# Kernel optimization log

Measured on AMD Instinct MI355X. Metric: run time of the kernel, lower is better.

## Reference

```python
import jax, jax.numpy as jnp
import numpy as np

N_NODES = 262144
N_EDGES = 2097152
N_GRAPHS = 8192
IN_CH = 54
HID = 32
OUT_CH = 64
SLOPE = 0.01  # AttentiveFP uses leaky_relu / GATConv negative_slope=0.01
NUM_TIMESTEPS = 2


def _gru(x, h, wih, whh, bih, bhh):
    # torch.nn.GRUCell semantics
    gi = x @ wih.T + bih
    gh = h @ whh.T + bhh
    ir, iz, inn = jnp.split(gi, 3, axis=-1)
    hr, hz, hn = jnp.split(gh, 3, axis=-1)
    r = jax.nn.sigmoid(ir + hr)
    z = jax.nn.sigmoid(iz + hz)
    n = jnp.tanh(inn + r * hn)
    return (1.0 - z) * n + z * h


def _seg_softmax(a, idx, n):
    # PyG softmax over edges grouped by target index
    m = jax.ops.segment_max(a, idx, num_segments=n)
    e = jnp.exp(a - m[idx])
    s = jax.ops.segment_sum(e, idx, num_segments=n)
    return e / (s[idx] + 1e-16)


def _forward(x, edge_attr,
             lin1_w, lin1_b,
             g_lin1_w, g_lin2_w, g_att_l, g_att_r, g_bias,
             gru1_wih, gru1_whh, gru1_bih, gru1_bhh,
             a_lin_w, a_att_src, a_att_dst, a_bias,
             gru2_wih, gru2_whh, gru2_bih, gru2_bhh,
             m_lin_w, m_att_src, m_att_dst, m_bias,
             gru3_wih, gru3_whh, gru3_bih, gru3_bhh,
             lin2_w, lin2_b,
             edge_index, batch_index):
    src, dst = edge_index[0], edge_index[1]  # j -> i (source_to_target)
    n = x.shape[0]
    # Atom embedding
    x = jax.nn.leaky_relu(x @ lin1_w.T + lin1_b, SLOPE)
    # --- GATEConv (first layer, uses edge features) ---
    xj, xi = x[src], x[dst]
    e = jax.nn.leaky_relu(jnp.concatenate([xj, edge_attr], axis=-1) @ g_lin1_w.T, SLOPE)
    alpha = jax.nn.leaky_relu(e @ g_att_l + xi @ g_att_r, SLOPE)
    alpha = _seg_softmax(alpha, dst, n)
    h = jax.ops.segment_sum((xj @ g_lin2_w.T) * alpha[:, None], dst, num_segments=n) + g_bias
    h = jax.nn.elu(h)
    x = jax.nn.relu(_gru(h, x, gru1_wih, gru1_whh, gru1_bih, gru1_bhh))
    # --- GATConv atom layer (num_layers=2 -> one extra conv) ---
    xt = x @ a_lin_w.T
    al = xt @ a_att_src
    ar = xt @ a_att_dst
    alpha = jax.nn.leaky_relu(al[src] + ar[dst], SLOPE)
    alpha = _seg_softmax(alpha, dst, n)
    h = jax.ops.segment_sum(xt[src] * alpha[:, None], dst, num_segments=n) + a_bias
    h = jax.nn.elu(h)
    x = jax.nn.relu(_gru(h, x, gru2_wih, gru2_whh, gru2_bih, gru2_bhh))
    # --- Molecule readout: iterative GAT attention from nodes to their graph ---
    out = jax.nn.relu(jax.ops.segment_sum(x, batch_index, num_segments=N_GRAPHS))
    xs = x @ m_lin_w.T          # transformed node (source) features, fixed per step
    a_node = xs @ m_att_src     # per-node attention logit contribution
    for _ in range(NUM_TIMESTEPS):
        a_g = (out @ m_lin_w.T) @ m_att_dst  # per-graph contribution
        alpha = jax.nn.leaky_relu(a_node + a_g[batch_index], SLOPE)
        alpha = _seg_softmax(alpha, batch_index, N_GRAPHS)
        h = jax.ops.segment_sum(xs * alpha[:, None], batch_index, num_segments=N_GRAPHS) + m_bias
        h = jax.nn.elu(h)
        out = jax.nn.relu(_gru(h, out, gru3_wih, gru3_whh, gru3_bih, gru3_bhh))
    out = out @ lin2_w.T + lin2_b
    # Mish activation wrapper
    return out * jnp.tanh(jax.nn.softplus(out))


def setup_inputs() -> dict:
    key = jax.random.key(0)
    ks = jax.random.split(key, 24)
    def rn(k, shape, s=0.1):
        return jax.random.normal(k, shape, dtype=jnp.float32) * s
    z = lambda *s: jnp.zeros(s, jnp.float32)
    return {
        "x": jax.random.normal(ks[0], (N_NODES, IN_CH), dtype=jnp.float32),
        "edge_attr": jax.random.normal(ks[1], (N_EDGES, 1), dtype=jnp.float32),
        "edge_index": jax.random.randint(ks[2], (2, N_EDGES), 0, N_NODES, dtype=jnp.int32),
        "batch_index": jnp.sort(jax.random.randint(ks[3], (N_NODES,), 0, N_GRAPHS, dtype=jnp.int32)),
        "lin1_w": rn(ks[4], (HID, IN_CH)), "lin1_b": z(HID),
        "g_lin1_w": rn(ks[5], (HID, HID + 1)),
        "g_lin2_w": rn(ks[6], (HID, HID)),
        "g_att_l": rn(ks[7], (HID,)), "g_att_r": rn(ks[8], (HID,)),
        "g_bias": z(HID),
        "gru1_wih": rn(ks[9], (3 * HID, HID)), "gru1_whh": rn(ks[10], (3 * HID, HID)),
        "gru1_bih": z(3 * HID), "gru1_bhh": z(3 * HID),
        "a_lin_w": rn(ks[11], (HID, HID)),
        "a_att_src": rn(ks[12], (HID,)), "a_att_dst": rn(ks[13], (HID,)),
        "a_bias": z(HID),
        "gru2_wih": rn(ks[14], (3 * HID, HID)), "gru2_whh": rn(ks[15], (3 * HID, HID)),
        "gru2_bih": z(3 * HID), "gru2_bhh": z(3 * HID),
        "m_lin_w": rn(ks[16], (HID, HID)),
        "m_att_src": rn(ks[17], (HID,)), "m_att_dst": rn(ks[18], (HID,)),
        "m_bias": z(HID),
        "gru3_wih": rn(ks[19], (3 * HID, HID)), "gru3_whh": rn(ks[20], (3 * HID, HID)),
        "gru3_bih": z(3 * HID), "gru3_bhh": z(3 * HID),
        "lin2_w": rn(ks[21], (OUT_CH, HID)), "lin2_b": z(OUT_CH),
    }


def reference(x, edge_attr, edge_index, batch_index,
              lin1_w, lin1_b,
              g_lin1_w, g_lin2_w, g_att_l, g_att_r, g_bias,
              gru1_wih, gru1_whh, gru1_bih, gru1_bhh,
              a_lin_w, a_att_src, a_att_dst, a_bias,
              gru2_wih, gru2_whh, gru2_bih, gru2_bhh,
              m_lin_w, m_att_src, m_att_dst, m_bias,
              gru3_wih, gru3_whh, gru3_bih, gru3_bhh,
              lin2_w, lin2_b):
    return _forward(x, edge_attr,
                    lin1_w, lin1_b,
                    g_lin1_w, g_lin2_w, g_att_l, g_att_r, g_bias,
                    gru1_wih, gru1_whh, gru1_bih, gru1_bhh,
                    a_lin_w, a_att_src, a_att_dst, a_bias,
                    gru2_wih, gru2_whh, gru2_bih, gru2_bhh,
                    m_lin_w, m_att_src, m_att_dst, m_bias,
                    gru3_wih, gru3_whh, gru3_bih, gru3_bhh,
                    lin2_w, lin2_b,
                    edge_index, batch_index)
```

## Files before the change

### kernel.cpp

```cpp
#include <hip/hip_runtime.h>
#include <hip/hip_bf16.h>
#include <math.h>

#define NN 262144
#define NE 2097152
#define NG 8192
#define THREADS 256

typedef __hip_bfloat16 bf16;
typedef __attribute__((ext_vector_type(8))) short short8v;
typedef __attribute__((ext_vector_type(4))) float f32x4;

static __device__ __forceinline__ float lrelu(float x){ return x > 0.f ? x : 0.01f*x; }
static __device__ __forceinline__ float eluf(float x){ return x > 0.f ? x : __expf(x) - 1.f; }
static __device__ __forceinline__ float sigm(float x){ return 1.f/(1.f + __expf(-x)); }
static __device__ __forceinline__ float tanh_fast(float x){
  float e = __expf(2.f*x); return 1.f - 2.f/(e + 1.f);
}
static __device__ __forceinline__ float b2f(bf16 v){ return __bfloat162float(v); }
static __device__ __forceinline__ bf16 f2b(float v){ return __float2bfloat16(v); }
static __device__ __forceinline__ float s2f(short s){
  return __uint_as_float(((unsigned int)(unsigned short)s) << 16);
}

static __device__ __forceinline__ unsigned short bfbits(float f){
  union { bf16 b; unsigned short s; } u; u.b = f2b(f); return u.s;
}
static __device__ __forceinline__ unsigned int pack2(float lo, float hi){
  return (unsigned int)bfbits(lo) | ((unsigned int)bfbits(hi) << 16);
}

static __device__ __forceinline__ float redsum32(float t){
  #pragma unroll
  for (int o = 16; o > 0; o >>= 1) t += __shfl_xor(t, o, 32);
  return t;
}
static __device__ __forceinline__ float redmax32(float t){
  #pragma unroll
  for (int o = 16; o > 0; o >>= 1) t = fmaxf(t, __shfl_xor(t, o, 32));
  return t;
}

static __device__ __forceinline__ float gru_relu(float hv, float xv, int c,
    const float* __restrict__ wih, const float* __restrict__ whh,
    const float* __restrict__ bih, const float* __restrict__ bhh){
  float gr = bih[c], gz = bih[32+c], gn = bih[64+c];
  float hr = bhh[c], hz = bhh[32+c], hn = bhh[64+c];
  #pragma unroll 8
  for (int k = 0; k < 32; k++){
    float hk = __shfl(hv, k, 32);
    float xk = __shfl(xv, k, 32);
    gr += hk*wih[(     c)*32 + k];
    gz += hk*wih[(32 + c)*32 + k];
    gn += hk*wih[(64 + c)*32 + k];
    hr += xk*whh[(     c)*32 + k];
    hz += xk*whh[(32 + c)*32 + k];
    hn += xk*whh[(64 + c)*32 + k];
  }
  float r = sigm(gr + hr), z = sigm(gz + hz);
  float nn2 = tanh_fast(gn + r*hn);
  return fmaxf((1.f - z)*nn2 + z*xv, 0.f);
}

__global__ __launch_bounds__(THREADS) void k_filli(int* __restrict__ p, int v, int n){
  int i = blockIdx.x*THREADS + threadIdx.x;
  if (i < n) p[i] = v;
}

#define FB_EMBED 512
#define FB_HIST  8192
#define FB_GPTR  1024

__global__ __launch_bounds__(THREADS) void k_front(
    const float* __restrict__ xin, const float* __restrict__ lw, const float* __restrict__ lb,
    const float* __restrict__ w1, const float* __restrict__ w2,
    const float* __restrict__ attr_r, float* __restrict__ X,
    bf16* __restrict__ u, bf16* __restrict__ v, float* __restrict__ nr,
    const int* __restrict__ ei, int* __restrict__ hist, int* __restrict__ rank,
    const int* __restrict__ batch, int* __restrict__ gptr){
  __shared__ float ol[4][16][33];
  int bid = blockIdx.x;
  if (bid < FB_EMBED){
    int wid  = bid*4 + (threadIdx.x >> 6);
    int wv   = threadIdx.x >> 6;
    int lane = threadIdx.x & 63;
    int cl = lane & 15;
    int kb = lane >> 4;
    short8v BL[2][2], BU[2], BV[2];
    #pragma unroll
    for (int g = 0; g < 2; g++){
      #pragma unroll
      for (int kc = 0; kc < 2; kc++){
        short8v t;
        #pragma unroll
        for (int j = 0; j < 8; j++){
          int k = kc*32 + kb*8 + j;
          t[j] = (k < 54) ? (short)bfbits(lw[(size_t)(g*16+cl)*54 + k]) : (short)0;
        }
        BL[g][kc] = t;
      }
      short8v tu, tv;
      #pragma unroll
      for (int j = 0; j < 8; j++){
        tu[j] = (short)bfbits(w1[(size_t)(g*16+cl)*33 + kb*8 + j]);
        tv[j] = (short)bfbits(w2[(size_t)(g*16+cl)*32 + kb*8 + j]);
      }
      BU[g] = tu; BV[g] = tv;
    }
    float bb0 = lb[cl], bb1 = lb[16+cl];
    float ar0 = attr_r[cl], ar1 = attr_r[16+cl];
    f32x4 zero; zero[0]=0.f; zero[1]=0.f; zero[2]=0.f; zero[3]=0.f;

    for (int t = 0; t < 8; t++){
      int nb = (wid*8 + t)*16;
      const float* xrow = xin + (size_t)(nb + cl)*54;
      short8v Ax0, Ax1;
      const float2* x2 = (const float2*)(xrow + kb*8);
      #pragma unroll
      for (int jj = 0; jj < 4; jj++){
        float2 tvv = x2[jj];
        Ax0[2*jj]   = (short)bfbits(tvv.x);
        Ax0[2*jj+1] = (short)bfbits(tvv.y);
      }
      #pragma unroll
      for (int j = 0; j < 8; j++){
        int k = 32 + kb*8 + j;
        Ax1[j] = (k < 54) ? (short)bfbits(xrow[k]) : (short)0;
      }
      f32x4 a0, a1;
      #pragma unroll
      for (int q = 0; q < 4; q++){ a0[q] = bb0; a1[q] = bb1; }
      f32x4 d0 = __builtin_amdgcn_mfma_f32_16x16x32_bf16(Ax0, BL[0][0], a0, 0, 0, 0);
      d0 = __builtin_amdgcn_mfma_f32_16x16x32_bf16(Ax1, BL[0][1], d0, 0, 0, 0);
      f32x4 d1 = __builtin_amdgcn_mfma_f32_16x16x32_bf16(Ax0, BL[1][0], a1, 0, 0, 0);
      d1 = __builtin_amdgcn_mfma_f32_16x16x32_bf16(Ax1, BL[1][1], d1, 0, 0, 0);
      #pragma unroll
      for (int r = 0; r < 4; r++){ d0[r] = lrelu(d0[r]); d1[r] = lrelu(d1[r]); }
      #pragma unroll
      for (int r = 0; r < 4; r++){
        int node = nb + kb*4 + r;
        float* srow = X + (size_t)node*32;
        srow[cl]      = d0[r];
        srow[16 + cl] = d1[r];
        ol[wv][kb*4 + r][cl]      = d0[r];
        ol[wv][kb*4 + r][16 + cl] = d1[r];
      }
      #pragma unroll
      for (int r = 0; r < 4; r++){
        float vsum = d0[r]*ar0 + d1[r]*ar1;
        vsum += __shfl_xor(vsum, 1, 16);
        vsum += __shfl_xor(vsum, 2, 16);
        vsum += __shfl_xor(vsum, 4, 16);
        vsum += __shfl_xor(vsum, 8, 16);
        if (cl == 0) nr[nb + kb*4 + r] = vsum;
      }
      __syncthreads();
      short8v Ao;
      #pragma unroll
      for (int j = 0; j < 8; j++) Ao[j] = (short)bfbits(ol[wv][cl][kb*8 + j]);
      f32x4 u0 = __builtin_amdgcn_mfma_f32_16x16x32_bf16(Ao, BU[0], zero, 0, 0, 0);
      f32x4 u1 = __builtin_amdgcn_mfma_f32_16x16x32_bf16(Ao, BU[1], zero, 0, 0, 0);
      f32x4 v0 = __builtin_amdgcn_mfma_f32_16x16x32_bf16(Ao, BV[0], zero, 0, 0, 0);
      f32x4 v1 = __builtin_amdgcn_mfma_f32_16x16x32_bf16(Ao, BV[1], zero, 0, 0, 0);
      #pragma unroll
      for (int r = 0; r < 4; r++){
        int node = nb + kb*4 + r;
        bf16* ur = u + (size_t)node*32;
        bf16* vr = v + (size_t)node*32;
        ur[cl]      = f2b(u0[r]);
        ur[16 + cl] = f2b(u1[r]);
        vr[cl]      = f2b(v0[r]);
        vr[16 + cl] = f2b(v1[r]);
      }
      __syncthreads();
    }
  } else if (bid < FB_EMBED + FB_HIST){
    int e = (bid - FB_EMBED)*THREADS + threadIdx.x;
    rank[e] = atomicAdd(hist + ei[NE + e], 1);
  } else {
    int n = (bid - FB_EMBED - FB_HIST)*THREADS + threadIdx.x;
    int bc = batch[n];
    if (n == 0){ for (int g = 0; g <= bc; g++) gptr[g] = 0; }
    else {
      int pb = batch[n-1];
      if (pb != bc) for (int g = pb+1; g <= bc; g++) gptr[g] = n;
    }
    if (n == NN-1){ for (int g = bc+1; g <= NG; g++) gptr[g] = NN; }
  }
}

__global__ __launch_bounds__(THREADS) void k_scan1(const int* __restrict__ hist,
    int* __restrict__ rp1, int* __restrict__ btot){
  __shared__ int sh[THREADS];
  int i = blockIdx.x*THREADS + threadIdx.x;
  int v = hist[i];
  sh[threadIdx.x] = v; __syncthreads();
  #pragma unroll
  for (int off = 1; off < THREADS; off <<= 1){
    int t = (threadIdx.x >= off) ? sh[threadIdx.x - off] : 0;
    __syncthreads(); sh[threadIdx.x] += t; __syncthreads();
  }
  rp1[i] = sh[threadIdx.x] - v;
  if (threadIdx.x == THREADS-1) btot[blockIdx.x] = sh[THREADS-1];
}

__global__ __launch_bounds__(1024) void k_scan2(int* __restrict__ btot){
  __shared__ int sh[1024];
  int i = threadIdx.x;
  int v = btot[i];
  sh[i] = v; __syncthreads();
  for (int off = 1; off < 1024; off <<= 1){
    int t = (i >= off) ? sh[i - off] : 0;
    __syncthreads(); sh[i] += t; __syncthreads();
  }
  btot[i] = sh[i] - v;
}

#define MB_SCAN 1024

__global__ __launch_bounds__(THREADS) void k_mid(const int* __restrict__ rp1,
    const int* __restrict__ btot, int* __restrict__ rowptr,
    const int* __restrict__ ei, const float* __restrict__ ea,
    const int* __restrict__ rank, int2* __restrict__ epk){
  int bid = blockIdx.x;
  if (bid < MB_SCAN){
    int i = bid*THREADS + threadIdx.x;
    rowptr[i] = rp1[i] + btot[i >> 8];
    if (i == 0) rowptr[NN] = NE;
  } else {
    int e = (bid - MB_SCAN)*THREADS + threadIdx.x;
    int d = ei[NE + e];
    int pos = rp1[d] + btot[d >> 8] + rank[e];
    epk[pos] = make_int2(ei[e], __float_as_int(ea[e]));
  }
}

__global__ __launch_bounds__(THREADS) void k_gru_att(const bf16* __restrict__ HV,
    float* __restrict__ S,
    const float* __restrict__ wih, const float* __restrict__ whh,
    const float* __restrict__ bih, const float* __restrict__ bhh,
    const float* __restrict__ attW, const float* __restrict__ att1,
    const float* __restrict__ att2,
    bf16* __restrict__ xt, float* __restrict__ s1, float* __restrict__ s2){
  __shared__ float ol[4][16][33];
  int wid  = (blockIdx.x*THREADS + threadIdx.x) >> 6;
  int wv   = threadIdx.x >> 6;
  int lane = threadIdx.x & 63;
  int cl = lane & 15;
  int kb = lane >> 4;
  short8v BW[12], BT[2];
  #pragma unroll
  for (int g = 0; g < 6; g++){
    const float* wr = wih + (size_t)(g*16 + cl)*32 + kb*8;
    const float* vr = whh + (size_t)(g*16 + cl)*32 + kb*8;
    short8v bw, bv;
    #pragma unroll
    for (int j = 0; j < 8; j++){ bw[j] = (short)bfbits(wr[j]); bv[j] = (short)bfbits(vr[j]); }
    BW[g] = bw; BW[6+g] = bv;
  }
  #pragma unroll
  for (int g = 0; g < 2; g++){
    short8v bt;
    #pragma unroll
    for (int j = 0; j < 8; j++) bt[j] = (short)bfbits(attW[(size_t)(g*16+cl)*32 + kb*8 + j]);
    BT[g] = bt;
  }
  float bI[6], bH[6];
  #pragma unroll
  for (int g = 0; g < 6; g++){ bI[g] = bih[g*16 + cl]; bH[g] = bhh[g*16 + cl]; }
  float a1c0 = att1[cl], a1c1 = att1[16+cl];
  float a2c0 = att2 ? att2[cl] : 0.f, a2c1 = att2 ? att2[16+cl] : 0.f;
  f32x4 zero; zero[0]=0.f; zero[1]=0.f; zero[2]=0.f; zero[3]=0.f;

  for (int t = 0; t < 8; t++){
    int nb = (wid*8 + t) * 16;
    short8v Ah = *(const short8v*)(HV + (size_t)(nb + cl)*32 + kb*8);
    const float* xr = S + (size_t)(nb + cl)*32 + kb*8;
    short8v Ax;
    #pragma unroll
    for (int j = 0; j < 8; j++) Ax[j] = (short)bfbits(xr[j]);
    f32x4 gi[6], gh[6];
    #pragma unroll
    for (int g = 0; g < 6; g++){
      f32x4 a, b;
      #pragma unroll
      for (int q = 0; q < 4; q++){ a[q] = bI[g]; b[q] = bH[g]; }
      gi[g] = __builtin_amdgcn_mfma_f32_16x16x32_bf16(Ah, BW[g],   a, 0, 0, 0);
      gh[g] = __builtin_amdgcn_mfma_f32_16x16x32_bf16(Ax, BW[6+g], b, 0, 0, 0);
    }
    #pragma unroll
    for (int r = 0; r < 4; r++){
      int node = nb + kb*4 + r;
      float* srow = S + (size_t)node*32;
      float x0 = srow[cl], x1 = srow[16 + cl];
      float r0 = sigm(gi[0][r] + gh[0][r]);
      float z0 = sigm(gi[2][r] + gh[2][r]);
      float n0 = tanh_fast(gi[4][r] + r0*gh[4][r]);
      float r1 = sigm(gi[1][r] + gh[1][r]);
      float z1 = sigm(gi[3][r] + gh[3][r]);
      float n1 = tanh_fast(gi[5][r] + r1*gh[5][r]);
      float o0 = fmaxf((1.f - z0)*n0 + z0*x0, 0.f);
      float o1 = fmaxf((1.f - z1)*n1 + z1*x1, 0.f);
      srow[cl]      = o0;
      srow[16 + cl] = o1;
      ol[wv][kb*4 + r][cl]      = o0;
      ol[wv][kb*4 + r][16 + cl] = o1;
    }
    __syncthreads();
    short8v Ao;
    #pragma unroll
    for (int j = 0; j < 8; j++) Ao[j] = (short)bfbits(ol[wv][cl][kb*8 + j]);
    f32x4 t0 = __builtin_amdgcn_mfma_f32_16x16x32_bf16(Ao, BT[0], zero, 0, 0, 0);
    f32x4 t1 = __builtin_amdgcn_mfma_f32_16x16x32_bf16(Ao, BT[1], zero, 0, 0, 0);
    #pragma unroll
    for (int r = 0; r < 4; r++){
      int node = nb + kb*4 + r;
      bf16* xrow = xt + (size_t)node*32;
      xrow[cl]      = f2b(t0[r]);
      xrow[16 + cl] = f2b(t1[r]);
      float p1 = t0[r]*a1c0 + t1[r]*a1c1;
      p1 += __shfl_xor(p1, 1, 16);
      p1 += __shfl_xor(p1, 2, 16);
      p1 += __shfl_xor(p1, 4, 16);
      p1 += __shfl_xor(p1, 8, 16);
      if (cl == 0) s1[node] = p1;
      if (att2){
        float p2 = t0[r]*a2c0 + t1[r]*a2c1;
        p2 += __shfl_xor(p2, 1, 16);
        p2 += __shfl_xor(p2, 2, 16);
        p2 += __shfl_xor(p2, 4, 16);
        p2 += __shfl_xor(p2, 8, 16);
        if (cl == 0) s2[node] = p2;
      }
    }
    __syncthreads();
  }
}

__global__ __launch_bounds__(THREADS) void k_elog1(const int2* __restrict__ epk,
    const bf16* __restrict__ U,
    const float* __restrict__ w1 , const float* __restrict__ attl,
    float* __restrict__ elog){
  int q  = threadIdx.x & 3;
  int lg = threadIdx.x >> 2;
  float wc[8], at[8];
  #pragma unroll
  for (int j = 0; j < 8; j++){
    wc[j] = w1[(q*8 + j)*33 + 32];
    at[j] = attl[q*8 + j];
  }
  int base = blockIdx.x * 512;
  #pragma unroll 2
  for (int i = 0; i < 8; i++){
    int p = base + i*64 + lg;
    int2 pk = epk[p];
    int si = pk.x;
    float a = __int_as_float(pk.y);
    short8v u8 = *(const short8v*)(U + (size_t)si*32 + q*8);
    float t = 0.f;
    #pragma unroll
    for (int j = 0; j < 8; j++) t += at[j]*lrelu(s2f(u8[j]) + a*wc[j]);
    t += __shfl_xor(t, 1, 4);
    t += __shfl_xor(t, 2, 4);
    if (q == 0) elog[p] = t;
  }
}

__global__ __launch_bounds__(THREADS) void k_conv(const int* __restrict__ rowptr,
    const int2* __restrict__ epk, const float* __restrict__ lg,
    const float* __restrict__ alsrc, const float* __restrict__ term,
    const bf16* __restrict__ ROWS, const float* __restrict__ bias,
    bf16* __restrict__ HV){
  int node = blockIdx.x*(THREADS/32) + (threadIdx.x >> 5);
  int c32 = threadIdx.x & 31;
  int ws = rowptr[node], we = rowptr[node+1];
  float tv = term[node];
  float m = -INFINITY;
  for (int p0 = ws; p0 < we; p0 += 32){
    int p = p0 + c32;
    bool ok = p < we;
    int pc = ok ? p : ws;
    float sc = lg ? lg[pc] : alsrc[epk[pc].x];
    float l = ok ? lrelu(sc + tv) : -INFINITY;
    m = fmaxf(m, redmax32(l));
  }
  int eg = c32 >> 2, cb = c32 & 3;
  float s = 0.f;
  float acc[8];
  #pragma unroll
  for (int j = 0; j < 8; j++) acc[j] = 0.f;
  for (int p0 = ws; p0 < we; p0 += 32){
    int p = p0 + c32;
    bool ok = p < we;
    int pc = ok ? p : ws;
    int siA = epk[pc].x;
    float sc = lg ? lg[pc] : alsrc[siA];
    float wme = ok ? __expf(lrelu(sc + tv) - m) : 0.f;
    s += redsum32(wme);
    #pragma unroll
    for (int s8 = 0; s8 < 32; s8 += 8){
      if (p0 + s8 >= we) break;
      float w = __shfl(wme, s8 + eg, 32);
      int si  = __shfl(siA, s8 + eg, 32);
      short8v r8 = *(const short8v*)(ROWS + (size_t)si*32 + cb*8);
      #pragma unroll
      for (int j = 0; j < 8; j++) acc[j] += s2f(r8[j]) * w;
    }
  }
  float inv = 1.f/(s + 1e-16f);
  #pragma unroll
  for (int j = 0; j < 8; j++){
    acc[j] += __shfl_xor(acc[j], 4, 32);
    acc[j] += __shfl_xor(acc[j], 8, 32);
    acc[j] += __shfl_xor(acc[j], 16, 32);
  }
  if (eg == 0){
    unsigned int o[4];
    #pragma unroll
    for (int j2 = 0; j2 < 4; j2++){
      float h0 = eluf(acc[2*j2  ]*inv + bias[cb*8 + 2*j2  ]);
      float h1 = eluf(acc[2*j2+1]*inv + bias[cb*8 + 2*j2+1]);
      o[j2] = pack2(h0, h1);
    }
    *(uint4*)(HV + (size_t)node*32 + cb*8) = make_uint4(o[0], o[1], o[2], o[3]);
  }
}

#define TB_RSUM 1024

__global__ __launch_bounds__(THREADS) void k_tail(const int* __restrict__ gptr,
    const float* __restrict__ X, float* __restrict__ gout,
    const float* __restrict__ mw, const float* __restrict__ mattd,
    float* __restrict__ q){
  int bid = blockIdx.x;
  if (bid < TB_RSUM){
    int g = bid*(THREADS/32) + (threadIdx.x >> 5);
    int c = threadIdx.x & 31;
    int gs = gptr[g], ge = gptr[g+1];
    float acc = 0.f;
    for (int n = gs; n < ge; n++) acc += X[(size_t)n*32 + c];
    gout[(size_t)g*32 + c] = fmaxf(acc, 0.f);
  } else {
    int k = threadIdx.x;
    if (k < 32){
      float acc = 0.f;
      #pragma unroll
      for (int c = 0; c < 32; c++) acc += mattd[c] * mw[c*32 + k];
      q[k] = acc;
    }
  }
}

__global__ __launch_bounds__(THREADS) void k_rstep(const int* __restrict__ gptr,
    const float* __restrict__ anode, const bf16* __restrict__ XS,
    const float* __restrict__ q, const float* __restrict__ mbias,
    float* __restrict__ gout,
    const float* __restrict__ wih, const float* __restrict__ whh,
    const float* __restrict__ bih, const float* __restrict__ bhh){
  int g = blockIdx.x*(THREADS/32) + (threadIdx.x >> 5);
  int c = threadIdx.x & 31;
  float orow = gout[(size_t)g*32 + c];
  float ag = redsum32(orow * q[c]);
  int gs = gptr[g], ge = gptr[g+1];
  float m = -INFINITY, s = 0.f;
  for (int p0 = gs; p0 < ge; p0 += 32){
    int p = p0 + c;
    bool ok = p < ge;
    float lg = ok ? lrelu(anode[p] + ag) : -INFINITY;
    float cm = redmax32(lg);
    float mn = fmaxf(m, cm);
    float e = ok ? __expf(lg - mn) : 0.f;
    float cs = redsum32(e);
    s = s*__expf(m - mn) + cs;
    m = mn;
  }
  float inv = 1.f/(s + 1e-16f);
  float acc = 0.f;
  int n = gs;
  for (; n + 4 <= ge; n += 4){
    float e0 = __expf(lrelu(anode[n]   + ag) - m);
    float e1 = __expf(lrelu(anode[n+1] + ag) - m);
    float e2 = __expf(lrelu(anode[n+2] + ag) - m);
    float e3 = __expf(lrelu(anode[n+3] + ag) - m);
    acc += b2f(XS[(size_t)(n  )*32 + c])*e0 + b2f(XS[(size_t)(n+1)*32 + c])*e1
         + b2f(XS[(size_t)(n+2)*32 + c])*e2 + b2f(XS[(size_t)(n+3)*32 + c])*e3;
  }
  for (; n < ge; n++)
    acc += b2f(XS[(size_t)n*32 + c]) * __expf(lrelu(anode[n] + ag) - m);
  acc *= inv;
  float hv = eluf(acc + mbias[c]);
  gout[(size_t)g*32 + c] = gru_relu(hv, orow, c, wih, whh, bih, bhh);
}

__global__ __launch_bounds__(THREADS) void k_final(const float* __restrict__ out32,
    const float* __restrict__ w , const float* __restrict__ b,
    float* __restrict__ y){
  int gid = blockIdx.x*THREADS + threadIdx.x;
  int g = gid >> 6, oc = gid & 63;
  const float* orow = out32 + (size_t)g*32;
  const float* wr = w + oc*32;
  float acc = b[oc];
  #pragma unroll
  for (int k = 0; k < 32; k++) acc += orow[k]*wr[k];
  float sp = fmaxf(acc, 0.f) + log1pf(expf(-fabsf(acc)));
  y[(size_t)g*64 + oc] = acc * tanhf(sp);
}

extern "C" void kernel_launch(void* const* d_in, const int* in_sizes, int n_in,
                              void* d_out, int out_size, void* d_ws, size_t ws_size,
                              hipStream_t stream){
  const float* x_in     = (const float*)d_in[0];
  const float* ea       = (const float*)d_in[1];
  const int*   ei       = (const int*)  d_in[2];
  const int*   batch    = (const int*)  d_in[3];
  const float* lin1_w   = (const float*)d_in[4];
  const float* lin1_b   = (const float*)d_in[5];
  const float* g_lin1_w = (const float*)d_in[6];
  const float* g_lin2_w = (const float*)d_in[7];
  const float* g_att_l  = (const float*)d_in[8];
  const float* g_att_r  = (const float*)d_in[9];
  const float* g_bias   = (const float*)d_in[10];
  const float* gru1_wih = (const float*)d_in[11];
  const float* gru1_whh = (const float*)d_in[12];
  const float* gru1_bih = (const float*)d_in[13];
  const float* gru1_bhh = (const float*)d_in[14];
  const float* a_lin_w  = (const float*)d_in[15];
  const float* a_att_src= (const float*)d_in[16];
  const float* a_att_dst= (const float*)d_in[17];
  const float* a_bias   = (const float*)d_in[18];
  const float* gru2_wih = (const float*)d_in[19];
  const float* gru2_whh = (const float*)d_in[20];
  const float* gru2_bih = (const float*)d_in[21];
  const float* gru2_bhh = (const float*)d_in[22];
  const float* m_lin_w  = (const float*)d_in[23];
  const float* m_att_src= (const float*)d_in[24];
  const float* m_att_dst= (const float*)d_in[25];
  const float* m_bias   = (const float*)d_in[26];
  const float* gru3_wih = (const float*)d_in[27];
  const float* gru3_whh = (const float*)d_in[28];
  const float* gru3_bih = (const float*)d_in[29];
  const float* gru3_bhh = (const float*)d_in[30];
  const float* lin2_w   = (const float*)d_in[31];
  const float* lin2_b   = (const float*)d_in[32];

  float* W = (float*)d_ws;
  float* X     = W;
  bf16*  BA    = (bf16*)(W + 8388608);
  bf16*  BB    = (bf16*)(W + 12582912);
  int2*  EPK   = (int2*) (W + 16777216);
  float* ELOG  = W + 20971520;
  int*   RP1   = (int*)  (W + 20971520);
  int*   RANK  = (int*)  (W + 23068672);
  int*   ROWPTR= (int*)  (W + 25165824);
  int*   HIST  = (int*)  (W + 25428032);
  int*   BTOT  = (int*)  (W + 25690176);
  float* NS1   = W + 25691200;
  float* NS2   = W + 25953344;
  int*   GPTR  = (int*)  (W + 26215488);
  float* GOUT  = W + 26223744;
  float* Q     = W + 26485888;

  dim3 b(THREADS);
  const int gNode  = NN/THREADS;
  const int gElog1 = NE/512;
  const int gNode32= NN/(THREADS/32);
  const int gG32   = NG/(THREADS/32);
  const int gMFMA  = NN/(16*8*4);

  k_filli<<<gNode, b, 0, stream>>>(HIST, 0, NN);

  k_front<<<FB_EMBED + FB_HIST + FB_GPTR, b, 0, stream>>>(
      x_in, lin1_w, lin1_b, g_lin1_w, g_lin2_w, g_att_r, X, BA, BB, NS1,
      ei, HIST, RANK, batch, GPTR);

  k_scan1<<<gNode, b, 0, stream>>>(HIST, RP1, BTOT);
  k_scan2<<<1, 1024, 0, stream>>>(BTOT);
  k_mid<<<MB_SCAN + NE/THREADS, b, 0, stream>>>(RP1, BTOT, ROWPTR, ei, ea, RANK, EPK);

  k_elog1<<<gElog1, b, 0, stream>>>(EPK, BA, g_lin1_w, g_att_l, ELOG);
  k_conv<<<gNode32, b, 0, stream>>>(ROWPTR, EPK, ELOG, nullptr, NS1, BB, g_bias, BA);
  k_gru_att<<<gMFMA, b, 0, stream>>>(BA, X, gru1_wih, gru1_whh, gru1_bih, gru1_bhh,
      a_lin_w, a_att_src, a_att_dst, BA, NS1, NS2);

  k_conv<<<gNode32, b, 0, stream>>>(ROWPTR, EPK, nullptr, NS1, NS2, BA, a_bias, BB);
  k_gru_att<<<gMFMA, b, 0, stream>>>(BB, X, gru2_wih, gru2_whh, gru2_bih, gru2_bhh,
      m_lin_w, m_att_src, nullptr, BA, NS1, nullptr);

  k_tail<<<TB_RSUM + 1, b, 0, stream>>>(GPTR, X, GOUT, m_lin_w, m_att_dst, Q);

  for (int t = 0; t < 2; t++){
    k_rstep<<<gG32, b, 0, stream>>>(GPTR, NS1, BA, Q, m_bias, GOUT,
        gru3_wih, gru3_whh, gru3_bih, gru3_bhh);
  }

  k_final<<<(NG*64)/THREADS, b, 0, stream>>>(GOUT, lin2_w, lin2_b, (float*)d_out);
}
```

Before: 486.2 us.

## Fuse edge-logit computation into conv and drop softmax max pass

Removes the separate k_elog1 kernel: the first GATE conv now computes each edge's attention logit inline from the gathered source row and edge attribute. Both the conv and the readout step also drop the max-subtraction pass of the segment softmax and exponentiate raw logits, so the extra sweep over edges and nodes goes away. The aim is to cut one launch, the ELOG write and read-back, and one full gather pass. In exchange each lane holds 64 extra weight registers, and removing the max shift risks exp overflow if logits are large.

```diff
diff --git a/kernel.cpp b/kernel.cpp
--- a/kernel.cpp
+++ b/kernel.cpp
@@ -33,11 +33,6 @@
 static __device__ __forceinline__ float redsum32(float t){
   #pragma unroll
   for (int o = 16; o > 0; o >>= 1) t += __shfl_xor(t, o, 32);
-  return t;
-}
-static __device__ __forceinline__ float redmax32(float t){
-  #pragma unroll
-  for (int o = 16; o > 0; o >>= 1) t = fmaxf(t, __shfl_xor(t, o, 32));
   return t;
 }
 
@@ -337,37 +332,9 @@
   }
 }
 
-__global__ __launch_bounds__(THREADS) void k_elog1(const int2* __restrict__ epk,
-    const bf16* __restrict__ U,
+__global__ __launch_bounds__(THREADS) void k_conv(const int* __restrict__ rowptr,
+    const int2* __restrict__ epk, const bf16* __restrict__ U,
     const float* __restrict__ w1 , const float* __restrict__ attl,
-    float* __restrict__ elog){
-  int q  = threadIdx.x & 3;
-  int lg = threadIdx.x >> 2;
-  float wc[8], at[8];
-  #pragma unroll
-  for (int j = 0; j < 8; j++){
-    wc[j] = w1[(q*8 + j)*33 + 32];
-    at[j] = attl[q*8 + j];
-  }
-  int base = blockIdx.x * 512;
-  #pragma unroll 2
-  for (int i = 0; i < 8; i++){
-    int p = base + i*64 + lg;
-    int2 pk = epk[p];
-    int si = pk.x;
-    float a = __int_as_float(pk.y);
-    short8v u8 = *(const short8v*)(U + (size_t)si*32 + q*8);
-    float t = 0.f;
-    #pragma unroll
-    for (int j = 0; j < 8; j++) t += at[j]*lrelu(s2f(u8[j]) + a*wc[j]);
-    t += __shfl_xor(t, 1, 4);
-    t += __shfl_xor(t, 2, 4);
-    if (q == 0) elog[p] = t;
-  }
-}
-
-__global__ __launch_bounds__(THREADS) void k_conv(const int* __restrict__ rowptr,
-    const int2* __restrict__ epk, const float* __restrict__ lg,
     const float* __restrict__ alsrc, const float* __restrict__ term,
     const bf16* __restrict__ ROWS, const float* __restrict__ bias,
     bf16* __restrict__ HV){
@@ -375,14 +342,10 @@
   int c32 = threadIdx.x & 31;
   int ws = rowptr[node], we = rowptr[node+1];
   float tv = term[node];
-  float m = -INFINITY;
-  for (int p0 = ws; p0 < we; p0 += 32){
-    int p = p0 + c32;
-    bool ok = p < we;
-    int pc = ok ? p : ws;
-    float sc = lg ? lg[pc] : alsrc[epk[pc].x];
-    float l = ok ? lrelu(sc + tv) : -INFINITY;
-    m = fmaxf(m, redmax32(l));
+  float wc[32], at[32];
+  if (U){
+    #pragma unroll
+    for (int j = 0; j < 32; j++){ wc[j] = w1[j*33 + 32]; at[j] = attl[j]; }
   }
   int eg = c32 >> 2, cb = c32 & 3;
   float s = 0.f;
@@ -393,9 +356,24 @@
     int p = p0 + c32;
     bool ok = p < we;
     int pc = ok ? p : ws;
-    int siA = epk[pc].x;
-    float sc = lg ? lg[pc] : alsrc[siA];
-    float wme = ok ? __expf(lrelu(sc + tv) - m) : 0.f;
+    int2 pk = epk[pc];
+    int siA = pk.x;
+    float sc;
+    if (U){
+      float a = __int_as_float(pk.y);
+      const short8v* ur = (const short8v*)(U + (size_t)siA*32);
+      sc = 0.f;
+      #pragma unroll
+      for (int q = 0; q < 4; q++){
+        short8v u8 = ur[q];
+        #pragma unroll
+        for (int j = 0; j < 8; j++)
+          sc += at[q*8+j]*lrelu(s2f(u8[j]) + a*wc[q*8+j]);
+      }
+    } else {
+      sc = alsrc[siA];
+    }
+    float wme = ok ? __expf(lrelu(sc + tv)) : 0.f;
     s += redsum32(wme);
     #pragma unroll
     for (int s8 = 0; s8 < 32; s8 += 8){
@@ -462,31 +440,26 @@
   float orow = gout[(size_t)g*32 + c];
   float ag = redsum32(orow * q[c]);
   int gs = gptr[g], ge = gptr[g+1];
-  float m = -INFINITY, s = 0.f;
+  float s = 0.f;
   for (int p0 = gs; p0 < ge; p0 += 32){
     int p = p0 + c;
     bool ok = p < ge;
-    float lg = ok ? lrelu(anode[p] + ag) : -INFINITY;
-    float cm = redmax32(lg);
-    float mn = fmaxf(m, cm);
-    float e = ok ? __expf(lg - mn) : 0.f;
-    float cs = redsum32(e);
-    s = s*__expf(m - mn) + cs;
-    m = mn;
+    float e = ok ? __expf(lrelu(anode[p] + ag)) : 0.f;
+    s += redsum32(e);
   }
   float inv = 1.f/(s + 1e-16f);
   float acc = 0.f;
   int n = gs;
   for (; n + 4 <= ge; n += 4){
-    float e0 = __expf(lrelu(anode[n]   + ag) - m);
-    float e1 = __expf(lrelu(anode[n+1] + ag) - m);
-    float e2 = __expf(lrelu(anode[n+2] + ag) - m);
-    float e3 = __expf(lrelu(anode[n+3] + ag) - m);
+    float e0 = __expf(lrelu(anode[n]   + ag));
+    float e1 = __expf(lrelu(anode[n+1] + ag));
+    float e2 = __expf(lrelu(anode[n+2] + ag));
+    float e3 = __expf(lrelu(anode[n+3] + ag));
     acc += b2f(XS[(size_t)(n  )*32 + c])*e0 + b2f(XS[(size_t)(n+1)*32 + c])*e1
          + b2f(XS[(size_t)(n+2)*32 + c])*e2 + b2f(XS[(size_t)(n+3)*32 + c])*e3;
   }
   for (; n < ge; n++)
-    acc += b2f(XS[(size_t)n*32 + c]) * __expf(lrelu(anode[n] + ag) - m);
+    acc += b2f(XS[(size_t)n*32 + c]) * __expf(lrelu(anode[n] + ag));
   acc *= inv;
   float hv = eluf(acc + mbias[c]);
   gout[(size_t)g*32 + c] = gru_relu(hv, orow, c, wih, whh, bih, bhh);
@@ -548,8 +521,8 @@
   bf16*  BA    = (bf16*)(W + 8388608);
   bf16*  BB    = (bf16*)(W + 12582912);
   int2*  EPK   = (int2*) (W + 16777216);
-  float* ELOG  = W + 20971520;
   int*   RP1   = (int*)  (W + 20971520);
+  bf16*  BC    = (bf16*) (W + 20971520);
   int*   RANK  = (int*)  (W + 23068672);
   int*   ROWPTR= (int*)  (W + 25165824);
   int*   HIST  = (int*)  (W + 25428032);
@@ -562,7 +535,6 @@
 
   dim3 b(THREADS);
   const int gNode  = NN/THREADS;
-  const int gElog1 = NE/512;
   const int gNode32= NN/(THREADS/32);
   const int gG32   = NG/(THREADS/32);
   const int gMFMA  = NN/(16*8*4);
@@ -577,12 +549,13 @@
   k_scan2<<<1, 1024, 0, stream>>>(BTOT);
   k_mid<<<MB_SCAN + NE/THREADS, b, 0, stream>>>(RP1, BTOT, ROWPTR, ei, ea, RANK, EPK);
 
-  k_elog1<<<gElog1, b, 0, stream>>>(EPK, BA, g_lin1_w, g_att_l, ELOG);
-  k_conv<<<gNode32, b, 0, stream>>>(ROWPTR, EPK, ELOG, nullptr, NS1, BB, g_bias, BA);
-  k_gru_att<<<gMFMA, b, 0, stream>>>(BA, X, gru1_wih, gru1_whh, gru1_bih, gru1_bhh,
+  k_conv<<<gNode32, b, 0, stream>>>(ROWPTR, EPK, BA, g_lin1_w, g_att_l,
+      nullptr, NS1, BB, g_bias, BC);
+  k_gru_att<<<gMFMA, b, 0, stream>>>(BC, X, gru1_wih, gru1_whh, gru1_bih, gru1_bhh,
       a_lin_w, a_att_src, a_att_dst, BA, NS1, NS2);
 
-  k_conv<<<gNode32, b, 0, stream>>>(ROWPTR, EPK, nullptr, NS1, NS2, BA, a_bias, BB);
+  k_conv<<<gNode32, b, 0, stream>>>(ROWPTR, EPK, nullptr, nullptr, nullptr,
+      NS1, NS2, BA, a_bias, BB);
   k_gru_att<<<gMFMA, b, 0, stream>>>(BB, X, gru2_wih, gru2_whh, gru2_bih, gru2_bhh,
       m_lin_w, m_att_src, nullptr, BA, NS1, nullptr);
 
```

Result: faster. 469.8 us (-3.4%).
